# Kernel optimization log

Measured on AMD Instinct MI355X. Metric: run time of the kernel, lower is better.

Reference implementation:

```python
import jax, jax.numpy as jnp
import numpy as np

TEMPERATURE = 8.0  # sqrt(d_k=64)
MASK_FILL = -1e10  # -10000000000.0 in the original


def setup_inputs() -> dict:
    key = jax.random.key(0)
    kq, kk, kv, ke, km = jax.random.split(key, 5)
    B, Lq, Lk, D = 16, 2048, 2048, 64
    q = jax.random.normal(kq, (B, Lq, D), dtype=jnp.float32)
    k = jax.random.normal(kk, (B, Lk, D), dtype=jnp.float32)
    v = jax.random.normal(kv, (B, Lk, D), dtype=jnp.float32)
    explain_weight = jax.random.uniform(ke, (B, Lq, Lk), dtype=jnp.float32)
    mask = jax.random.randint(km, (B, Lq, Lk), 0, 2).astype(bool)
    return {"q": q, "k": k, "v": v, "explain_weight": explain_weight, "mask": mask}


def reference(q, k, v, explain_weight, mask):
    # attn = bmm(q, k^T) / temperature, masked fill, softmax over keys
    attn = jnp.einsum("bqd,bkd->bqk", q, k) / TEMPERATURE
    attn = jnp.where(mask, MASK_FILL, attn)
    attn = jax.nn.softmax(attn, axis=2)
    # dropout is identity in eval mode; post-softmax explain reweighting
    attn = attn * explain_weight
    output = jnp.einsum("bqk,bkd->bqd", attn, v)
    return (output, attn)
```

## Files before the change

### kernel.cpp

```cpp
#include <hip/hip_runtime.h>
#include <cstdint>
#include <cstddef>

#define NB 16
#define NL 2048
#define ND 64
#define QT 16
#define NW 8
#define NTHREADS (NW * 64)
#define SLICE (NL / NW)
#define NT (SLICE / 16)
#define ROWU 1026
#define ELSU (QT * ROWU)
#define LDSB (ELSU * 4)

typedef __attribute__((ext_vector_type(8))) short bf16x8;
typedef __attribute__((ext_vector_type(4))) float f32x4;
typedef __attribute__((ext_vector_type(4))) int i32x4;
typedef __attribute__((ext_vector_type(4))) unsigned short u16x4;
typedef __attribute__((ext_vector_type(2))) unsigned int u32x2;
typedef __attribute__((ext_vector_type(4))) unsigned int u32x4;
typedef unsigned short u16;

#define MFMA __builtin_amdgcn_mfma_f32_16x16x32_bf16

__device__ __forceinline__ u16 f2bf(float x) {
  union { float f; uint32_t u; } v; v.f = x;
  uint32_t r = v.u + 0x7FFFu + ((v.u >> 16) & 1u);
  return (u16)(r >> 16);
}
__device__ __forceinline__ float bfhi2f(uint32_t w) {
  union { uint32_t u; float f; } v; v.u = w & 0xFFFF0000u; return v.f;
}
__device__ __forceinline__ float bflo2f(uint32_t w) {
  union { uint32_t u; float f; } v; v.u = w << 16; return v.f;
}
__device__ __forceinline__ int swzb(int cb) { return cb ^ (((cb >> 7) & 7) << 4); }

template <int MODE>
__device__ __forceinline__ uint32_t mnib(const void* __restrict__ m, size_t i) {
  if constexpr (MODE == 1) {
    const uint32_t x = __builtin_nontemporal_load((const uint32_t*)((const uint8_t*)m + i));
    return (x | (x >> 7) | (x >> 14) | (x >> 21)) & 0xFu;
  } else if constexpr (MODE == 0) {
    const i32x4 x = __builtin_nontemporal_load(((const i32x4*)((const int*)m + i)));
    return (uint32_t)(x[0] != 0) | ((uint32_t)(x[1] != 0) << 1) |
           ((uint32_t)(x[2] != 0) << 2) | ((uint32_t)(x[3] != 0) << 3);
  } else if constexpr (MODE == 2) {
    const f32x4 x = __builtin_nontemporal_load(((const f32x4*)((const float*)m + i)));
    return (uint32_t)(x[0] != 0.f) | ((uint32_t)(x[1] != 0.f) << 1) |
           ((uint32_t)(x[2] != 0.f) << 2) | ((uint32_t)(x[3] != 0.f) << 3);
  } else {
    const uint32_t* p = (const uint32_t*)m + 2 * i;
    return (uint32_t)(p[0] != 0u) | ((uint32_t)(p[2] != 0u) << 1) |
           ((uint32_t)(p[4] != 0u) << 2) | ((uint32_t)(p[6] != 0u) << 3);
  }
}

template <bool WS>
__device__ __forceinline__ void loadKfrag(const float* __restrict__ k,
                                          const u16* __restrict__ kb,
                                          int b, int row, int kg,
                                          bf16x8& b0, bf16x8& b1) {
  if constexpr (WS) {
    const u16* kp = kb + ((size_t)(b * NL + row)) * ND + kg * 8;
    b0 = *(const bf16x8*)kp;
    b1 = *(const bf16x8*)(kp + 32);
  } else {
    const float* kp = k + ((size_t)(b * NL + row)) * ND + kg * 8;
#pragma unroll
    for (int i = 0; i < 8; ++i) {
      b0[i] = (short)f2bf(kp[i]);
      b1[i] = (short)f2bf(kp[i + 32]);
    }
  }
}

template <int MMODE, bool WS>
__device__ __forceinline__ void attn_core(
    const float* __restrict__ q, const float* __restrict__ k,
    const float* __restrict__ v, const float* __restrict__ ew,
    const void* __restrict__ mask,
    const u16* __restrict__ qs, const u16* __restrict__ kb,
    const u16* __restrict__ vt, const uint32_t* __restrict__ mb,
    float* __restrict__ out, float* __restrict__ attn,
    uint32_t* __restrict__ els, float* __restrict__ rsums) {
  const int tid = threadIdx.x;
  const int lane = tid & 63;
  const int w = tid >> 6;
  const int fr = lane & 15;
  const int kg = lane >> 4;

  const int bid = blockIdx.x;
  const int swzid = (bid & 7) * ((NB * (NL / QT)) / 8) + (bid >> 3);
  const int b = swzid >> 7;
  const int q0 = (swzid & 127) * QT;
  const int cbase = w * SLICE;
  const size_t bq = (size_t)b * NL + q0;
  const size_t mrow0 = bq * NL;
  const size_t lrow = mrow0 + (size_t)fr * NL + (size_t)(cbase + 4 * kg);

  bf16x8 a0, a1;
  if constexpr (WS) {
    const u16* qp = qs + (bq + fr) * ND + kg * 8;
    a0 = *(const bf16x8*)qp;
    a1 = *(const bf16x8*)(qp + 32);
  } else {
    const float* qp = q + (bq + fr) * ND + kg * 8;
#pragma unroll
    for (int i = 0; i < 8; ++i) {
      a0[i] = (short)f2bf(qp[i] * 0.125f);
      a1[i] = (short)f2bf(qp[i + 32] * 0.125f);
    }
  }

  uint32_t mw[8];
  if constexpr (WS) {
    const uint32_t* mbr = mb + (bq + fr) * (NL / 32) + (cbase >> 5);
#pragma unroll
    for (int u = 0; u < 8; ++u) mw[u] = mbr[u];
  }

  float rs = 0.f;
#pragma unroll
  for (int ti = 0; ti < NT; ++ti) {
    const int c0 = cbase + ti * 16;
    bf16x8 b0, b1;
    loadKfrag<WS>(k, kb, b, c0 + fr, kg, b0, b1);
    f32x4 s = {0.f, 0.f, 0.f, 0.f};
    s = MFMA(b0, a0, s, 0, 0, 0);
    s = MFMA(b1, a1, s, 0, 0, 0);
    uint32_t nib;
    if constexpr (WS) nib = (mw[ti >> 1] >> (16 * (ti & 1) + 4 * kg)) & 0xFu;
    else              nib = mnib<MMODE>(mask, lrow + (size_t)(ti * 16));
    const float e0 = (nib & 1u) ? 0.f : __expf(s[0]);
    const float e1 = (nib & 2u) ? 0.f : __expf(s[1]);
    const float e2 = (nib & 4u) ? 0.f : __expf(s[2]);
    const float e3 = (nib & 8u) ? 0.f : __expf(s[3]);
    rs += (e0 + e1) + (e2 + e3);
    u32x2 ep;
    ep[0] = (uint32_t)f2bf(e0) | ((uint32_t)f2bf(e1) << 16);
    ep[1] = (uint32_t)f2bf(e2) | ((uint32_t)f2bf(e3) << 16);
    *(u32x2*)(els + fr * ROWU + (swzb((c0 + 4 * kg) * 2) >> 2)) = ep;
  }
  rs += __shfl_xor(rs, 16, 64);
  rs += __shfl_xor(rs, 32, 64);
  if (lane < 16) rsums[w * QT + fr] = rs;
  __syncthreads();

#pragma unroll
  for (int half = 0; half < 2; ++half) {
    const int rr = 2 * w + half;
    float inv = 0.f;
#pragma unroll
    for (int ww = 0; ww < NW; ++ww) inv += rsums[ww * QT + rr];
    inv = 1.0f / inv;
    const size_t gb = (bq + rr) * NL + 4 * lane;
    const float* ewp = ew + gb;
    float* atp = attn + gb;
    uint32_t* lrp = els + rr * ROWU;
    f32x4 w4[8];
    u32x2 el8[8];
#pragma unroll
    for (int s2 = 0; s2 < 8; ++s2)
      w4[s2] = __builtin_nontemporal_load((const f32x4*)(ewp + 256 * s2));
#pragma unroll
    for (int s2 = 0; s2 < 8; ++s2)
      el8[s2] = *(const u32x2*)(lrp + (swzb(512 * s2 + 8 * lane) >> 2));
#pragma unroll
    for (int s2 = 0; s2 < 8; ++s2) {
      f32x4 p;
      p[0] = bflo2f(el8[s2][0]) * inv * w4[s2][0];
      p[1] = bfhi2f(el8[s2][0]) * inv * w4[s2][1];
      p[2] = bflo2f(el8[s2][1]) * inv * w4[s2][2];
      p[3] = bfhi2f(el8[s2][1]) * inv * w4[s2][3];
      __builtin_nontemporal_store(p, (f32x4*)(atp + 256 * s2));
      u32x2 pp;
      pp[0] = (uint32_t)f2bf(p[0]) | ((uint32_t)f2bf(p[1]) << 16);
      pp[1] = (uint32_t)f2bf(p[2]) | ((uint32_t)f2bf(p[3]) << 16);
      *(u32x2*)(lrp + (swzb(512 * s2 + 8 * lane) >> 2)) = pp;
    }
  }
  __syncthreads();

  f32x4 oA[4] = {{0.f,0.f,0.f,0.f},{0.f,0.f,0.f,0.f},{0.f,0.f,0.f,0.f},{0.f,0.f,0.f,0.f}};
#pragma unroll
  for (int gi = 0; gi < NT / 2; ++gi) {
    union { u32x4 u; bf16x8 v8; } pu;
    pu.u = *(const u32x4*)(els + fr * ROWU + (swzb((cbase + 32 * gi + 8 * kg) * 2) >> 2));
    const bf16x8 pa = pu.v8;
    const int kk = cbase + gi * 32 + kg * 8;
    if constexpr (WS) {
      const u16* vp = vt + ((size_t)(b * ND + fr)) * NL + kk;
      oA[0] = MFMA(pa, *(const bf16x8*)(vp),           oA[0], 0, 0, 0);
      oA[1] = MFMA(pa, *(const bf16x8*)(vp + 16 * NL), oA[1], 0, 0, 0);
      oA[2] = MFMA(pa, *(const bf16x8*)(vp + 32 * NL), oA[2], 0, 0, 0);
      oA[3] = MFMA(pa, *(const bf16x8*)(vp + 48 * NL), oA[3], 0, 0, 0);
    } else {
#pragma unroll
      for (int dt = 0; dt < 4; ++dt) {
        bf16x8 vf;
#pragma unroll
        for (int i = 0; i < 8; ++i)
          vf[i] = (short)f2bf(v[((size_t)(b * NL + kk + i)) * ND + dt * 16 + fr]);
        oA[dt] = MFMA(pa, vf, oA[dt], 0, 0, 0);
      }
    }
  }
  __syncthreads();

  float* osta = (float*)els;
  f32x4 acc = {0.f, 0.f, 0.f, 0.f};
  const int rrr = tid >> 4;
  const int d4 = (tid & 15) * 4;
#pragma unroll
  for (int round = 0; round < NW / 2; ++round) {
    if ((w >> 1) == round) {
      float* od = osta + (w & 1) * (QT * ND);
#pragma unroll
      for (int dt = 0; dt < 4; ++dt)
#pragma unroll
        for (int j = 0; j < 4; ++j)
          od[(4 * kg + j) * ND + dt * 16 + fr] = oA[dt][j];
    }
    __syncthreads();
    if (tid < QT * ND / 4) {
      acc += *(const f32x4*)(osta + rrr * ND + d4) +
             *(const f32x4*)(osta + QT * ND + rrr * ND + d4);
    }
    __syncthreads();
  }
  if (tid < QT * ND / 4)
    *(f32x4*)(out + (bq + rrr) * ND + d4) = acc;
}

__global__ void __launch_bounds__(NTHREADS, 4)
attn_ws(const float* __restrict__ q, const float* __restrict__ k,
        const float* __restrict__ v, const float* __restrict__ ew,
        const u16* __restrict__ qs, const u16* __restrict__ kb,
        const u16* __restrict__ vt, const uint32_t* __restrict__ mb,
        float* __restrict__ out, float* __restrict__ attn) {
  extern __shared__ uint32_t els[];
  __shared__ float rsums[NW * QT];
  attn_core<0, true>(q, k, v, ew, nullptr, qs, kb, vt, mb, out, attn, els, rsums);
}

__global__ void __launch_bounds__(NTHREADS, 4)
attn_fb(const float* __restrict__ q, const float* __restrict__ k,
        const float* __restrict__ v, const float* __restrict__ ew,
        const void* __restrict__ mask,
        float* __restrict__ out, float* __restrict__ attn) {
  extern __shared__ uint32_t els[];
  __shared__ float rsums[NW * QT];
  __shared__ int s_mode;
  if (threadIdx.x < 64) {
    const uint32_t x = ((const uint32_t*)mask)[threadIdx.x];
    const int all01 = __all(x <= 1u);
    const int allf  = __all(x == 0u || x == 0x3F800000u);
    const int oddz  = __all(((threadIdx.x & 1) == 0) || (x == 0u));
    if (threadIdx.x == 0) s_mode = all01 ? (oddz ? 3 : 0) : (allf ? 2 : 1);
  }
  __syncthreads();
  switch (s_mode) {
    case 0:  attn_core<0, false>(q, k, v, ew, mask, nullptr, nullptr, nullptr, nullptr, out, attn, els, rsums); break;
    case 1:  attn_core<1, false>(q, k, v, ew, mask, nullptr, nullptr, nullptr, nullptr, out, attn, els, rsums); break;
    case 2:  attn_core<2, false>(q, k, v, ew, mask, nullptr, nullptr, nullptr, nullptr, out, attn, els, rsums); break;
    default: attn_core<3, false>(q, k, v, ew, mask, nullptr, nullptr, nullptr, nullptr, out, attn, els, rsums); break;
  }
}

__global__ void __launch_bounds__(256)
prep_qk(const float* __restrict__ q, const float* __restrict__ k,
        u16* __restrict__ qs, u16* __restrict__ kb) {
  const size_t NQ4 = (size_t)NB * NL * ND / 4;
  const size_t i = (size_t)blockIdx.x * 256 + threadIdx.x;
  f32x4 val;
  u16* dst;
  if (i < NQ4) {
    val = ((const f32x4*)q)[i];
    val *= 0.125f;
    dst = qs + i * 4;
  } else {
    val = ((const f32x4*)k)[i - NQ4];
    dst = kb + (i - NQ4) * 4;
  }
  u16x4 o;
#pragma unroll
  for (int j = 0; j < 4; ++j) o[j] = f2bf(val[j]);
  *(u16x4*)dst = o;
}

__global__ void __launch_bounds__(256)
prep_vt(const float* __restrict__ v, u16* __restrict__ vt) {
  __shared__ float t[64 * 68];
  const int b = blockIdx.y;
  const int k0 = blockIdx.x * 64;
  const int tid = threadIdx.x;
  const int rr = tid >> 4;
  const int c4 = (tid & 15) * 4;
#pragma unroll
  for (int i = 0; i < 4; ++i) {
    const int r = rr + 16 * i;
    const f32x4 val = *(const f32x4*)(v + ((size_t)(b * NL + k0 + r)) * ND + c4);
    *(f32x4*)(t + r * 68 + c4) = val;
  }
  __syncthreads();
#pragma unroll
  for (int i = 0; i < 4; ++i) {
    const int d = rr + 16 * i;
    u16x4 o;
#pragma unroll
    for (int j = 0; j < 4; ++j) o[j] = f2bf(t[(c4 + j) * 68 + d]);
    *(u16x4*)(vt + ((size_t)(b * ND + d)) * NL + k0 + c4) = o;
  }
}

__global__ void __launch_bounds__(256)
prep_mask(const void* __restrict__ mask, uint32_t* __restrict__ mb) {
  __shared__ int pm;
  if (threadIdx.x < 64) {
    const uint32_t x = ((const uint32_t*)mask)[threadIdx.x];
    const int all01 = __all(x <= 1u);
    const int allf  = __all(x == 0u || x == 0x3F800000u);
    const int oddz  = __all(((threadIdx.x & 1) == 0) || (x == 0u));
    if (threadIdx.x == 0) pm = all01 ? (oddz ? 3 : 0) : (allf ? 2 : 1);
  }
  __syncthreads();
  const int mode = pm;
  const size_t t = (size_t)blockIdx.x * 256 + threadIdx.x;
  uint32_t bits = 0;
  if (mode == 1) {
    const u32x4 x0 = *(((const u32x4*)mask) + t * 2);
    const u32x4 x1 = *(((const u32x4*)mask) + t * 2 + 1);
#pragma unroll
    for (int i = 0; i < 4; ++i)
#pragma unroll
      for (int by = 0; by < 4; ++by) {
        bits |= (((x0[i] >> (8 * by)) & 0xFFu) ? 1u : 0u) << (i * 4 + by);
        bits |= (((x1[i] >> (8 * by)) & 0xFFu) ? 1u : 0u) << (16 + i * 4 + by);
      }
  } else if (mode == 0 || mode == 2) {
#pragma unroll
    for (int c = 0; c < 8; ++c) {
      const u32x4 x = *(((const u32x4*)mask) + t * 8 + c);
#pragma unroll
      for (int i = 0; i < 4; ++i) bits |= (x[i] ? 1u : 0u) << (c * 4 + i);
    }
  } else {
    const uint32_t* p = (const uint32_t*)mask;
#pragma unroll
    for (int i = 0; i < 32; ++i) bits |= (p[2 * (t * 32 + i)] ? 1u : 0u) << i;
  }
  mb[t] = bits;
}

extern "C" void kernel_launch(void* const* d_in, const int* in_sizes, int n_in,
                              void* d_out, int out_size, void* d_ws, size_t ws_size,
                              hipStream_t stream) {
  const float* q    = (const float*)d_in[0];
  const float* k    = (const float*)d_in[1];
  const float* v    = (const float*)d_in[2];
  const float* ew   = (const float*)d_in[3];
  const void*  mask = d_in[4];
  float* out  = (float*)d_out;
  float* attn = out + (size_t)NB * NL * ND;

  const size_t QE = (size_t)NB * NL * ND;
  const size_t MBW = (size_t)NB * NL * (NL / 32);
  u16* qs = (u16*)d_ws;
  u16* kb = qs + QE;
  u16* vt = kb + QE;
  uint32_t* mb = (uint32_t*)(vt + QE);

  (void)hipFuncSetAttribute(reinterpret_cast<const void*>(attn_ws),
                            hipFuncAttributeMaxDynamicSharedMemorySize, LDSB);
  (void)hipFuncSetAttribute(reinterpret_cast<const void*>(attn_fb),
                            hipFuncAttributeMaxDynamicSharedMemorySize, LDSB);

  dim3 grid(NB * (NL / QT));
  if (ws_size >= 3 * QE * sizeof(u16) + MBW * sizeof(uint32_t)) {
    prep_qk<<<dim3((unsigned)(2 * QE / 4 / 256)), 256, 0, stream>>>(q, k, qs, kb);
    prep_vt<<<dim3(NL / 64, NB), 256, 0, stream>>>(v, vt);
    prep_mask<<<dim3((unsigned)(MBW / 256)), 256, 0, stream>>>(mask, mb);
    attn_ws<<<grid, NTHREADS, LDSB, stream>>>(q, k, v, ew, qs, kb, vt, mb, out, attn);
  } else {
    attn_fb<<<grid, NTHREADS, LDSB, stream>>>(q, k, v, ew, mask, out, attn);
  }
}
```

Before: 255.0 us.

## Prefetch explain weights before QK phase and remap normalize to per-warp column slices

```diff
diff --git a/kernel.cpp b/kernel.cpp
--- a/kernel.cpp
+++ b/kernel.cpp
@@ -99,6 +99,12 @@
   const size_t bq = (size_t)b * NL + q0;
   const size_t mrow0 = bq * NL;
   const size_t lrow = mrow0 + (size_t)fr * NL + (size_t)(cbase + 4 * kg);
+
+  const float* ewbase = ew + bq * NL + cbase + 4 * lane;
+  f32x4 ewr[16];
+#pragma unroll
+  for (int r = 0; r < 16; ++r)
+    ewr[r] = __builtin_nontemporal_load((const f32x4*)(ewbase + (size_t)r * NL));
 
   bf16x8 a0, a1;
   if constexpr (WS) {
@@ -146,42 +152,33 @@
   rs += __shfl_xor(rs, 16, 64);
   rs += __shfl_xor(rs, 32, 64);
   if (lane < 16) rsums[w * QT + fr] = rs;
-  __syncthreads();
-
-#pragma unroll
-  for (int half = 0; half < 2; ++half) {
-    const int rr = 2 * w + half;
-    float inv = 0.f;
-#pragma unroll
-    for (int ww = 0; ww < NW; ++ww) inv += rsums[ww * QT + rr];
-    inv = 1.0f / inv;
-    const size_t gb = (bq + rr) * NL + 4 * lane;
-    const float* ewp = ew + gb;
-    float* atp = attn + gb;
-    uint32_t* lrp = els + rr * ROWU;
-    f32x4 w4[8];
-    u32x2 el8[8];
-#pragma unroll
-    for (int s2 = 0; s2 < 8; ++s2)
-      w4[s2] = __builtin_nontemporal_load((const f32x4*)(ewp + 256 * s2));
-#pragma unroll
-    for (int s2 = 0; s2 < 8; ++s2)
-      el8[s2] = *(const u32x2*)(lrp + (swzb(512 * s2 + 8 * lane) >> 2));
-#pragma unroll
-    for (int s2 = 0; s2 < 8; ++s2) {
-      f32x4 p;
-      p[0] = bflo2f(el8[s2][0]) * inv * w4[s2][0];
-      p[1] = bfhi2f(el8[s2][0]) * inv * w4[s2][1];
-      p[2] = bflo2f(el8[s2][1]) * inv * w4[s2][2];
-      p[3] = bfhi2f(el8[s2][1]) * inv * w4[s2][3];
-      __builtin_nontemporal_store(p, (f32x4*)(atp + 256 * s2));
-      u32x2 pp;
-      pp[0] = (uint32_t)f2bf(p[0]) | ((uint32_t)f2bf(p[1]) << 16);
-      pp[1] = (uint32_t)f2bf(p[2]) | ((uint32_t)f2bf(p[3]) << 16);
-      *(u32x2*)(lrp + (swzb(512 * s2 + 8 * lane) >> 2)) = pp;
-    }
-  }
-  __syncthreads();
+
+#pragma unroll
+  for (int r = 0; r < 16; ++r) asm volatile("" : "+v"(ewr[r]));
+  __syncthreads();
+
+  float invf = 0.f;
+#pragma unroll
+  for (int ww = 0; ww < NW; ++ww) invf += rsums[ww * QT + fr];
+  invf = 1.0f / invf;
+
+  float* atb = attn + bq * NL + cbase + 4 * lane;
+  const int lofs = swzb((cbase + 4 * lane) * 2) >> 2;
+#pragma unroll
+  for (int r = 0; r < 16; ++r) {
+    const u32x2 el = *(const u32x2*)(els + r * ROWU + lofs);
+    const float inv_r = __shfl(invf, r, 64);
+    f32x4 p;
+    p[0] = bflo2f(el[0]) * inv_r * ewr[r][0];
+    p[1] = bfhi2f(el[0]) * inv_r * ewr[r][1];
+    p[2] = bflo2f(el[1]) * inv_r * ewr[r][2];
+    p[3] = bfhi2f(el[1]) * inv_r * ewr[r][3];
+    __builtin_nontemporal_store(p, (f32x4*)(atb + (size_t)r * NL));
+    u32x2 pp;
+    pp[0] = (uint32_t)f2bf(p[0]) | ((uint32_t)f2bf(p[1]) << 16);
+    pp[1] = (uint32_t)f2bf(p[2]) | ((uint32_t)f2bf(p[3]) << 16);
+    *(u32x2*)(els + r * ROWU + lofs) = pp;
+  }
 
   f32x4 oA[4] = {{0.f,0.f,0.f,0.f},{0.f,0.f,0.f,0.f},{0.f,0.f,0.f,0.f},{0.f,0.f,0.f,0.f}};
 #pragma unroll
```

Measured after the change: 249.4 us. 1.02x faster.
